# Optimization experiments

Hardware: AMD Instinct MI355X
Metric: run time of the kernel (lower is better)

The kernel has to match this reference:

```python
import jax, jax.numpy as jnp
import numpy as np

D_MODEL = 1024
NUM_HEADS = 16
HEAD_DIM = D_MODEL // NUM_HEADS


def setup_inputs() -> dict:
    key = jax.random.key(0)
    k_x, k_wqkv, k_bqkv, k_wo, k_bo = jax.random.split(key, 5)
    B, T = 2, 2048
    x = jax.random.normal(k_x, (B, T, D_MODEL), dtype=jnp.float32)
    # flax Dense default: lecun_normal kernel, zero bias; we use scaled normal for kernels
    w_qkv = jax.random.normal(k_wqkv, (D_MODEL, 3 * D_MODEL), dtype=jnp.float32) / np.sqrt(D_MODEL)
    b_qkv = jnp.zeros((3 * D_MODEL,), dtype=jnp.float32)
    w_out = jax.random.normal(k_wo, (D_MODEL, D_MODEL), dtype=jnp.float32) / np.sqrt(D_MODEL)
    b_out = jnp.zeros((D_MODEL,), dtype=jnp.float32)
    return {"x": x, "w_qkv": w_qkv, "b_qkv": b_qkv, "w_out": w_out, "b_out": b_out}


def reference(x, w_qkv, b_qkv, w_out, b_out):
    B, T, C = x.shape
    H, D = NUM_HEADS, HEAD_DIM
    qkv = x @ w_qkv + b_qkv                      # [B,T,3C]
    q, k, v = jnp.split(qkv, 3, axis=-1)         # each [B,T,C]

    def split_heads(t):
        return t.reshape(B, T, H, D).transpose(0, 2, 1, 3)  # [B,H,T,D]

    q, k, v = split_heads(q), split_heads(k), split_heads(v)
    attn = jnp.einsum('bhqd,bhkd->bhqk', q, k) / jnp.sqrt(jnp.float32(D))
    attn = jax.nn.softmax(attn, axis=-1)
    out = jnp.einsum('bhqk,bhkd->bhqd', attn, v)  # [B,H,T,D]
    out = out.transpose(0, 2, 1, 3).reshape(B, T, H * D)
    return out @ w_out + b_out
```

## Files before the change

kernel.cpp:

```cpp
#include <hip/hip_runtime.h>
#include <math.h>

#define D_MODEL 1024
#define NHEAD   16
#define HDIM    64
#define BATCH   2
#define SEQ     2048
#define M_TOTAL (BATCH*SEQ)

typedef _Float16 f16;
typedef _Float16 f16x4 __attribute__((ext_vector_type(4)));
typedef _Float16 f16x8 __attribute__((ext_vector_type(8)));
typedef float    f32x4 __attribute__((ext_vector_type(4)));

#if __has_builtin(__builtin_amdgcn_exp2f)
#define EXP2F(x) __builtin_amdgcn_exp2f(x)
#else
#define EXP2F(x) exp2f(x)
#endif

#define QSCALE 0.18033688011112042f

__device__ __forceinline__ void gl2lds16(const f16* g, f16* l) {
    __builtin_amdgcn_global_load_lds(
        (const __attribute__((address_space(1))) void*)g,
        (__attribute__((address_space(3))) void*)l,
        16, 0, 0);
}

__global__ __launch_bounds__(256) void convert_x_kernel(
    const float* __restrict__ x, f16* __restrict__ xh, int n4)
{
    int i = blockIdx.x * 256 + threadIdx.x;
    if (i >= n4) return;
    float4 v = ((const float4*)x)[i];
    f16x4 hv = {(f16)v.x, (f16)v.y, (f16)v.z, (f16)v.w};
    *(f16x4*)&xh[(size_t)i * 4] = hv;
}

__global__ __launch_bounds__(256) void convert_wt_kernel(
    const float* __restrict__ W, f16* __restrict__ Wth, int K, int N)
{
    __shared__ float tile[64][65];
    const int n0 = blockIdx.x * 64, k0 = blockIdx.y * 64;
    const int tx = threadIdx.x & 15, ty = threadIdx.x >> 4;
    #pragma unroll
    for (int i = 0; i < 4; ++i) {
        float4 v = *(const float4*)&W[(size_t)(k0 + ty + 16*i) * N + n0 + tx*4];
        tile[ty + 16*i][tx*4 + 0] = v.x;
        tile[ty + 16*i][tx*4 + 1] = v.y;
        tile[ty + 16*i][tx*4 + 2] = v.z;
        tile[ty + 16*i][tx*4 + 3] = v.w;
    }
    __syncthreads();
    #pragma unroll
    for (int i = 0; i < 4; ++i) {
        int n = ty + 16*i;
        f16x4 hv = {(f16)tile[tx*4 + 0][n], (f16)tile[tx*4 + 1][n],
                    (f16)tile[tx*4 + 2][n], (f16)tile[tx*4 + 3][n]};
        *(f16x4*)&Wth[(size_t)(n0 + n) * K + k0 + tx*4] = hv;
    }
}

__global__ __launch_bounds__(256) void gemm_qkv_mfma(
    const f16* __restrict__ Ahg, const f16* __restrict__ Bhg,
    const float* __restrict__ bias,
    f16* __restrict__ Qf, f16* __restrict__ Kf, f16* __restrict__ Vt)
{
    const int K = 1024;
    const int flat = blockIdx.x;
    const int xcd  = flat & 7;
    const int idx  = flat >> 3;
    const int m_blk = (xcd >> 1) * 8  + (idx & 7);
    const int n_blk = (xcd & 1) * 12 + (idx >> 3);
    const int n0 = n_blk * 128;
    const int m0 = m_blk * 128;
    const int tid  = threadIdx.x;
    const int lane = tid & 63;
    const int wave = tid >> 6;
    const int quad = lane >> 4;
    const int txl  = lane & 15;
    const int wm = (wave >> 1) * 64;
    const int wn = (wave & 1) * 64;

    __shared__ __align__(16) f16 sAh[128*64];
    __shared__ __align__(16) f16 sBh[128*64];

    f32x4 acc[4][4];
    #pragma unroll
    for (int i = 0; i < 4; ++i)
        #pragma unroll
        for (int j = 0; j < 4; ++j) { f32x4 z = {0.f,0.f,0.f,0.f}; acc[i][j] = z; }

    for (int kt = 0; kt < K; kt += 64) {
        __syncthreads();
        #pragma unroll
        for (int it = 0; it < 4; ++it) {
            int f = it*256 + tid;
            int r = f >> 3;
            int gc = (f & 7) ^ (r & 7);
            gl2lds16(&Ahg[(size_t)(m0 + r) * K + kt + gc*8], &sAh[f*8]);
            gl2lds16(&Bhg[(size_t)(n0 + r) * K + kt + gc*8], &sBh[f*8]);
        }
        __syncthreads();

        #pragma unroll
        for (int ks = 0; ks < 2; ++ks) {
            f16x8 ah[4], bh[4];
            #pragma unroll
            for (int i = 0; i < 4; ++i) {
                int r = wm + 16*i + txl;
                ah[i] = *(const f16x8*)&sAh[(r*8 + ((ks*4 + quad) ^ (r & 7))) * 8];
            }
            #pragma unroll
            for (int j = 0; j < 4; ++j) {
                int r = wn + 16*j + txl;
                bh[j] = *(const f16x8*)&sBh[(r*8 + ((ks*4 + quad) ^ (r & 7))) * 8];
            }
            #pragma unroll
            for (int j = 0; j < 4; ++j)
                #pragma unroll
                for (int i = 0; i < 4; ++i)
                    acc[i][j] = __builtin_amdgcn_mfma_f32_16x16x32_f16(ah[i], bh[j], acc[i][j], 0,0,0);
        }
    }

    #pragma unroll
    for (int j = 0; j < 4; ++j) {
        int n = n0 + wn + 16*j + txl;
        float bv = bias[n];
        int which = n >> 10;
        int h = (n >> 6) & 15;
        int d = n & 63;
        #pragma unroll
        for (int i = 0; i < 4; ++i) {
            int m0i = m0 + wm + 16*i + quad*4;
            int bb  = m0i >> 11;
            int t0  = m0i & (SEQ - 1);
            if (which == 2) {
                f16x4 pw = {(f16)(acc[i][j][0] + bv), (f16)(acc[i][j][1] + bv),
                            (f16)(acc[i][j][2] + bv), (f16)(acc[i][j][3] + bv)};
                *(f16x4*)&Vt[((size_t)(bb*NHEAD + h) * HDIM + d) * SEQ + t0] = pw;
            } else {
                #pragma unroll
                for (int rr = 0; rr < 4; ++rr) {
                    float v = acc[i][j][rr] + bv;
                    if (which == 0)
                        Qf[((size_t)(bb*NHEAD + h) * SEQ + t0 + rr) * HDIM + d] = (f16)(v * QSCALE);
                    else
                        Kf[((size_t)(bb*NHEAD + h) * SEQ + t0 + rr) * HDIM + d] = (f16)v;
                }
            }
        }
    }
}

__global__ __launch_bounds__(256, 4) void attn_mfma(
    const f16* __restrict__ Qf, const f16* __restrict__ Kf,
    const f16* __restrict__ Vt, f16* __restrict__ Oat)
{
    const int flat = blockIdx.x;
    const int xcd  = flat & 7;
    const int idx  = flat >> 3;
    const int bh = xcd*4 + (idx >> 5);
    const int qt = idx & 31;
    const int b  = bh >> 4;
    const int h  = bh & 15;
    const int tid  = threadIdx.x;
    const int lane = tid & 63;
    const int wave = tid >> 6;
    const int quad = lane >> 4;
    const int txl  = lane & 15;
    const int qh = wave >> 1;
    const int kh = wave & 1;

    __shared__ __align__(16) char smem[40960];
    f16* sQ  = (f16*)smem;
    f16* sKb = (f16*)(smem + 8*1024);
    f16* sVb = (f16*)(smem + 24*1024);
    float* sL      = (float*)smem;
    float* scratch = (float*)(smem + 8*1024);

    const f16* Qg = Qf + (size_t)bh * SEQ * HDIM + (size_t)qt * 64 * HDIM;
    const f16* Kg = Kf + (size_t)bh * SEQ * HDIM;
    const f16* Vg = Vt + (size_t)bh * HDIM * SEQ;

    #pragma unroll
    for (int it = 0; it < 2; ++it) {
        int f = it*256 + tid;
        int r = f >> 3;
        int gc = (f & 7) ^ (r & 7);
        gl2lds16(&Qg[(size_t)r * HDIM + gc*8], &sQ[f*8]);
        gl2lds16(&Kg[(size_t)r * HDIM + gc*8], &sKb[f*8]);
        gl2lds16(&Vg[(size_t)r * SEQ + gc*8], &sVb[f*8]);
    }
    __syncthreads();

    f16x8 bq[2][2];
    #pragma unroll
    for (int i = 0; i < 2; ++i) {
        int row = qh*32 + i*16 + txl;
        #pragma unroll
        for (int dc = 0; dc < 2; ++dc) {
            int cp = (dc*4 + quad) ^ (row & 7);
            bq[i][dc] = *(const f16x8*)&sQ[(row*8 + cp) * 8];
        }
    }
    __syncthreads();

    f32x4 oacc[2][4];
    f32x4 lmf[2];
    const f16x4 vones = {(f16)1.f, (f16)1.f, (f16)1.f, (f16)1.f};
    #pragma unroll
    for (int i = 0; i < 2; ++i) {
        f32x4 z = {0.f,0.f,0.f,0.f};
        lmf[i] = z;
        #pragma unroll
        for (int jn = 0; jn < 4; ++jn) oacc[i][jn] = z;
    }

    const int NT = SEQ / 64;
    #pragma unroll 2
    for (int t = 0; t < NT; ++t) {
        const f16* sKc = sKb + (t & 1) * 4096;
        const f16* sVc = sVb + (t & 1) * 4096;
        if (t + 1 < NT) {
            f16* sKn = sKb + ((t + 1) & 1) * 4096;
            f16* sVn = sVb + ((t + 1) & 1) * 4096;
            int kt2 = (t + 1) * 64;
            #pragma unroll
            for (int it = 0; it < 2; ++it) {
                int f = it*256 + tid;
                int r = f >> 3;
                int gc = (f & 7) ^ (r & 7);
                gl2lds16(&Kg[(size_t)(kt2 + r) * HDIM + gc*8], &sKn[f*8]);
                gl2lds16(&Vg[(size_t)r * SEQ + kt2 + gc*8], &sVn[f*8]);
            }
        }

        __builtin_amdgcn_s_setprio(1);
        #pragma unroll
        for (int kg = 0; kg < 2; ++kg) {
            int krow = kh*32 + kg*16 + txl;
            f16x8 aK0 = *(const f16x8*)&sKc[(krow*8 + ((quad    ) ^ (krow & 7))) * 8];
            f16x8 aK1 = *(const f16x8*)&sKc[(krow*8 + ((quad + 4) ^ (krow & 7))) * 8];
            f16x4 bV[4];
            #pragma unroll
            for (int jn = 0; jn < 4; ++jn) {
                int d = jn*16 + txl;
                int slot = (kh*4 + kg*2 + (quad >> 1)) ^ (d & 7);
                bV[jn] = *(const f16x4*)&sVc[d*64 + slot*8 + (quad & 1)*4];
            }
            #pragma unroll
            for (int i = 0; i < 2; ++i) {
                f32x4 s = {0.f,0.f,0.f,0.f};
                s = __builtin_amdgcn_mfma_f32_16x16x32_f16(aK0, bq[i][0], s, 0,0,0);
                s = __builtin_amdgcn_mfma_f32_16x16x32_f16(aK1, bq[i][1], s, 0,0,0);
                float p0 = EXP2F(s[0]), p1 = EXP2F(s[1]);
                float p2 = EXP2F(s[2]), p3 = EXP2F(s[3]);
                f16x4 pa = {(f16)p0, (f16)p1, (f16)p2, (f16)p3};
                lmf[i] = __builtin_amdgcn_mfma_f32_16x16x16f16(pa, vones, lmf[i], 0,0,0);
                #pragma unroll
                for (int jn = 0; jn < 4; ++jn)
                    oacc[i][jn] = __builtin_amdgcn_mfma_f32_16x16x16f16(pa, bV[jn], oacc[i][jn], 0,0,0);
            }
        }
        __builtin_amdgcn_s_setprio(0);
        __syncthreads();
    }

    if (txl == 0) {
        *(f32x4*)&sL[wave*32 +  0 + quad*4] = lmf[0];
        *(f32x4*)&sL[wave*32 + 16 + quad*4] = lmf[1];
    }

    const int s_  = tid >> 3;
    const int sqh = s_ >> 4;
    const int sql = s_ & 15;
    const int d8  = (tid & 7) * 8;

    #pragma unroll
    for (int i = 0; i < 2; ++i) {
        #pragma unroll
        for (int jn = 0; jn < 4; ++jn) {
            #pragma unroll
            for (int rr = 0; rr < 4; ++rr)
                scratch[wave*1088 + (quad*4 + rr)*68 + jn*16 + txl] = oacc[i][jn][rr];
        }
        __syncthreads();
        float l = sL[(sqh*2)*32 + i*16 + sql] + sL[(sqh*2 + 1)*32 + i*16 + sql];
        float rl = 1.0f / l;
        f32x4 o0a = *(const f32x4*)&scratch[(sqh*2    )*1088 + sql*68 + d8];
        f32x4 o0b = *(const f32x4*)&scratch[(sqh*2    )*1088 + sql*68 + d8 + 4];
        f32x4 o1a = *(const f32x4*)&scratch[(sqh*2 + 1)*1088 + sql*68 + d8];
        f32x4 o1b = *(const f32x4*)&scratch[(sqh*2 + 1)*1088 + sql*68 + d8 + 4];
        f16x8 ow;
        ow[0] = (f16)((o0a[0] + o1a[0]) * rl);
        ow[1] = (f16)((o0a[1] + o1a[1]) * rl);
        ow[2] = (f16)((o0a[2] + o1a[2]) * rl);
        ow[3] = (f16)((o0a[3] + o1a[3]) * rl);
        ow[4] = (f16)((o0b[0] + o1b[0]) * rl);
        ow[5] = (f16)((o0b[1] + o1b[1]) * rl);
        ow[6] = (f16)((o0b[2] + o1b[2]) * rl);
        ow[7] = (f16)((o0b[3] + o1b[3]) * rl);
        int q = qt*64 + sqh*32 + i*16 + sql;
        *(f16x8*)&Oat[(size_t)(b*SEQ + q) * D_MODEL + h*HDIM + d8] = ow;
        __syncthreads();
    }
}

__global__ __launch_bounds__(256) void gemm_out_mfma(
    const f16* __restrict__ Ag, const f16* __restrict__ Bhg,
    const float* __restrict__ bias, float* __restrict__ Cg)
{
    const int K = 1024, N = 1024;
    const int flat = blockIdx.x;
    const int xcd  = flat & 7;
    const int idx  = flat >> 3;
    const int m0 = (xcd*8 + (idx & 7)) * 64;
    const int n0 = (idx >> 3) * 64;
    const int tid  = threadIdx.x;
    const int lane = tid & 63;
    const int wave = tid >> 6;
    const int quad = lane >> 4;
    const int txl  = lane & 15;
    const int wm = (wave >> 1) * 32;
    const int wn = (wave & 1) * 32;

    __shared__ __align__(16) f16 sA[64*64];
    __shared__ __align__(16) f16 sB[64*64];

    f32x4 acc[2][2];
    #pragma unroll
    for (int i = 0; i < 2; ++i)
        #pragma unroll
        for (int j = 0; j < 2; ++j) { f32x4 z = {0.f,0.f,0.f,0.f}; acc[i][j] = z; }

    for (int kt = 0; kt < K; kt += 64) {
        __syncthreads();
        #pragma unroll
        for (int it = 0; it < 2; ++it) {
            int f = it*256 + tid;
            int r = f >> 3;
            int gc = (f & 7) ^ (r & 7);
            gl2lds16(&Ag[(size_t)(m0 + r) * K + kt + gc*8], &sA[f*8]);
            gl2lds16(&Bhg[(size_t)(n0 + r) * K + kt + gc*8], &sB[f*8]);
        }
        __syncthreads();

        #pragma unroll
        for (int ks = 0; ks < 2; ++ks) {
            f16x8 a[2], bb[2];
            #pragma unroll
            for (int i = 0; i < 2; ++i) {
                int r = wm + 16*i + txl;
                a[i] = *(const f16x8*)&sA[(r*8 + ((ks*4 + quad) ^ (r & 7))) * 8];
            }
            #pragma unroll
            for (int j = 0; j < 2; ++j) {
                int r = wn + 16*j + txl;
                bb[j] = *(const f16x8*)&sB[(r*8 + ((ks*4 + quad) ^ (r & 7))) * 8];
            }
            #pragma unroll
            for (int j = 0; j < 2; ++j)
                #pragma unroll
                for (int i = 0; i < 2; ++i)
                    acc[i][j] = __builtin_amdgcn_mfma_f32_16x16x32_f16(a[i], bb[j], acc[i][j], 0,0,0);
        }
    }

    #pragma unroll
    for (int j = 0; j < 2; ++j) {
        int n = n0 + wn + 16*j + txl;
        float bv = bias[n];
        #pragma unroll
        for (int i = 0; i < 2; ++i) {
            #pragma unroll
            for (int rr = 0; rr < 4; ++rr) {
                int m = m0 + wm + 16*i + quad*4 + rr;
                Cg[(size_t)m * N + n] = acc[i][j][rr] + bv;
            }
        }
    }
}

extern "C" void kernel_launch(void* const* d_in, const int* in_sizes, int n_in,
                              void* d_out, int out_size, void* d_ws, size_t ws_size,
                              hipStream_t stream) {
    (void)in_sizes; (void)n_in; (void)out_size; (void)ws_size;
    const float* x     = (const float*)d_in[0];
    const float* w_qkv = (const float*)d_in[1];
    const float* b_qkv = (const float*)d_in[2];
    const float* w_out = (const float*)d_in[3];
    const float* b_out = (const float*)d_in[4];
    float* out = (float*)d_out;

    const size_t MB = 1024*1024;
    char* ws = (char*)d_ws;
    f16* xh  = (f16*)(ws + 0*MB);
    f16* Wth = (f16*)(ws + 8*MB);
    f16* Woh = (f16*)(ws + 14*MB);
    f16* Qf  = (f16*)(ws + 16*MB);
    f16* Kf  = (f16*)(ws + 24*MB);
    f16* Vt  = (f16*)(ws + 32*MB);
    f16* Oat = (f16*)(ws + 40*MB);

    convert_x_kernel<<<4096, 256, 0, stream>>>(x, xh, M_TOTAL*D_MODEL/4);
    convert_wt_kernel<<<dim3(48, 16), 256, 0, stream>>>(w_qkv, Wth, 1024, 3072);
    convert_wt_kernel<<<dim3(16, 16), 256, 0, stream>>>(w_out, Woh, 1024, 1024);
    gemm_qkv_mfma<<<768, 256, 0, stream>>>(xh, Wth, b_qkv, Qf, Kf, Vt);
    attn_mfma<<<1024, 256, 0, stream>>>(Qf, Kf, Vt, Oat);
    gemm_out_mfma<<<1024, 256, 0, stream>>>(Oat, Woh, b_out, out);
}
```

Measured before the change: 182.6 us.

## Use 16x16x32 MFMA for PV in attention and fuse conversion kernels

```diff
diff --git a/kernel.cpp b/kernel.cpp
--- a/kernel.cpp
+++ b/kernel.cpp
@@ -28,21 +28,31 @@
         16, 0, 0);
 }
 
-__global__ __launch_bounds__(256) void convert_x_kernel(
-    const float* __restrict__ x, f16* __restrict__ xh, int n4)
-{
-    int i = blockIdx.x * 256 + threadIdx.x;
-    if (i >= n4) return;
-    float4 v = ((const float4*)x)[i];
-    f16x4 hv = {(f16)v.x, (f16)v.y, (f16)v.z, (f16)v.w};
-    *(f16x4*)&xh[(size_t)i * 4] = hv;
-}
-
-__global__ __launch_bounds__(256) void convert_wt_kernel(
-    const float* __restrict__ W, f16* __restrict__ Wth, int K, int N)
+__global__ __launch_bounds__(256) void convert_fused_kernel(
+    const float* __restrict__ x, f16* __restrict__ xh,
+    const float* __restrict__ w_qkv, f16* __restrict__ Wth,
+    const float* __restrict__ w_out, f16* __restrict__ Woh)
 {
     __shared__ float tile[64][65];
-    const int n0 = blockIdx.x * 64, k0 = blockIdx.y * 64;
+    const int bid = blockIdx.x;
+    if (bid < 4096) {
+        int i = bid * 256 + threadIdx.x;
+        float4 v = ((const float4*)x)[i];
+        f16x4 hv = {(f16)v.x, (f16)v.y, (f16)v.z, (f16)v.w};
+        *(f16x4*)&xh[(size_t)i * 4] = hv;
+        return;
+    }
+    const float* W; f16* Wt; int N, n0, k0;
+    if (bid < 4096 + 768) {
+        int b2 = bid - 4096;
+        W = w_qkv; Wt = Wth; N = 3072;
+        n0 = (b2 % 48) * 64; k0 = (b2 / 48) * 64;
+    } else {
+        int b3 = bid - 4864;
+        W = w_out; Wt = Woh; N = 1024;
+        n0 = (b3 & 15) * 64; k0 = (b3 >> 4) * 64;
+    }
+    const int K = 1024;
     const int tx = threadIdx.x & 15, ty = threadIdx.x >> 4;
     #pragma unroll
     for (int i = 0; i < 4; ++i) {
@@ -58,7 +68,7 @@
         int n = ty + 16*i;
         f16x4 hv = {(f16)tile[tx*4 + 0][n], (f16)tile[tx*4 + 1][n],
                     (f16)tile[tx*4 + 2][n], (f16)tile[tx*4 + 3][n]};
-        *(f16x4*)&Wth[(size_t)(n0 + n) * K + k0 + tx*4] = hv;
+        *(f16x4*)&Wt[(size_t)(n0 + n) * K + k0 + tx*4] = hv;
     }
 }
 
@@ -208,9 +218,17 @@
     }
     __syncthreads();
 
+    const int pr0 = kh*32 + ((txl & 12) << 1) + (txl & 3);
+    const int pr1 = pr0 + 4;
+    const int c00 = quad ^ (pr0 & 7);
+    const int c01 = (quad + 4) ^ (pr0 & 7);
+    const int c10 = quad ^ (pr1 & 7);
+    const int c11 = (quad + 4) ^ (pr1 & 7);
+
     f32x4 oacc[2][4];
     f32x4 lmf[2];
-    const f16x4 vones = {(f16)1.f, (f16)1.f, (f16)1.f, (f16)1.f};
+    const f16x8 vones8 = {(f16)1.f, (f16)1.f, (f16)1.f, (f16)1.f,
+                          (f16)1.f, (f16)1.f, (f16)1.f, (f16)1.f};
     #pragma unroll
     for (int i = 0; i < 2; ++i) {
         f32x4 z = {0.f,0.f,0.f,0.f};
@@ -239,30 +257,34 @@
         }
 
         __builtin_amdgcn_s_setprio(1);
-        #pragma unroll
-        for (int kg = 0; kg < 2; ++kg) {
-            int krow = kh*32 + kg*16 + txl;
-            f16x8 aK0 = *(const f16x8*)&sKc[(krow*8 + ((quad    ) ^ (krow & 7))) * 8];
-            f16x8 aK1 = *(const f16x8*)&sKc[(krow*8 + ((quad + 4) ^ (krow & 7))) * 8];
-            f16x4 bV[4];
+        {
+            f16x8 aK00 = *(const f16x8*)&sKc[(pr0*8 + c00) * 8];
+            f16x8 aK01 = *(const f16x8*)&sKc[(pr0*8 + c01) * 8];
+            f16x8 aK10 = *(const f16x8*)&sKc[(pr1*8 + c10) * 8];
+            f16x8 aK11 = *(const f16x8*)&sKc[(pr1*8 + c11) * 8];
+            f16x8 bV[4];
             #pragma unroll
             for (int jn = 0; jn < 4; ++jn) {
                 int d = jn*16 + txl;
-                int slot = (kh*4 + kg*2 + (quad >> 1)) ^ (d & 7);
-                bV[jn] = *(const f16x4*)&sVc[d*64 + slot*8 + (quad & 1)*4];
+                bV[jn] = *(const f16x8*)&sVc[d*64 + (((kh*4 + quad) ^ (d & 7)) * 8)];
             }
             #pragma unroll
             for (int i = 0; i < 2; ++i) {
-                f32x4 s = {0.f,0.f,0.f,0.f};
-                s = __builtin_amdgcn_mfma_f32_16x16x32_f16(aK0, bq[i][0], s, 0,0,0);
-                s = __builtin_amdgcn_mfma_f32_16x16x32_f16(aK1, bq[i][1], s, 0,0,0);
-                float p0 = EXP2F(s[0]), p1 = EXP2F(s[1]);
-                float p2 = EXP2F(s[2]), p3 = EXP2F(s[3]);
-                f16x4 pa = {(f16)p0, (f16)p1, (f16)p2, (f16)p3};
-                lmf[i] = __builtin_amdgcn_mfma_f32_16x16x16f16(pa, vones, lmf[i], 0,0,0);
+                f32x4 z = {0.f,0.f,0.f,0.f};
+                f32x4 sA = __builtin_amdgcn_mfma_f32_16x16x32_f16(aK00, bq[i][0], z, 0,0,0);
+                sA = __builtin_amdgcn_mfma_f32_16x16x32_f16(aK01, bq[i][1], sA, 0,0,0);
+                f32x4 sB = __builtin_amdgcn_mfma_f32_16x16x32_f16(aK10, bq[i][0], z, 0,0,0);
+                sB = __builtin_amdgcn_mfma_f32_16x16x32_f16(aK11, bq[i][1], sB, 0,0,0);
+                float p0 = EXP2F(sA[0]), p1 = EXP2F(sA[1]);
+                float p2 = EXP2F(sA[2]), p3 = EXP2F(sA[3]);
+                float p4 = EXP2F(sB[0]), p5 = EXP2F(sB[1]);
+                float p6 = EXP2F(sB[2]), p7 = EXP2F(sB[3]);
+                f16x8 pa = {(f16)p0, (f16)p1, (f16)p2, (f16)p3,
+                            (f16)p4, (f16)p5, (f16)p6, (f16)p7};
+                lmf[i] = __builtin_amdgcn_mfma_f32_16x16x32_f16(pa, vones8, lmf[i], 0,0,0);
                 #pragma unroll
                 for (int jn = 0; jn < 4; ++jn)
-                    oacc[i][jn] = __builtin_amdgcn_mfma_f32_16x16x16f16(pa, bV[jn], oacc[i][jn], 0,0,0);
+                    oacc[i][jn] = __builtin_amdgcn_mfma_f32_16x16x32_f16(pa, bV[jn], oacc[i][jn], 0,0,0);
             }
         }
         __builtin_amdgcn_s_setprio(0);
@@ -405,9 +427,7 @@
     f16* Vt  = (f16*)(ws + 32*MB);
     f16* Oat = (f16*)(ws + 40*MB);
 
-    convert_x_kernel<<<4096, 256, 0, stream>>>(x, xh, M_TOTAL*D_MODEL/4);
-    convert_wt_kernel<<<dim3(48, 16), 256, 0, stream>>>(w_qkv, Wth, 1024, 3072);
-    convert_wt_kernel<<<dim3(16, 16), 256, 0, stream>>>(w_out, Woh, 1024, 1024);
+    convert_fused_kernel<<<5120, 256, 0, stream>>>(x, xh, w_qkv, Wth, w_out, Woh);
     gemm_qkv_mfma<<<768, 256, 0, stream>>>(xh, Wth, b_qkv, Qf, Kf, Vt);
     attn_mfma<<<1024, 256, 0, stream>>>(Qf, Kf, Vt, Oat);
     gemm_out_mfma<<<1024, 256, 0, stream>>>(Oat, Woh, b_out, out);
```

After: 171.7 us. 5.9% less time.
